# Optimization experiments

Hardware: AMD Instinct MI355X
Metric: run time of the kernel (lower is better)

The kernel has to match this reference:

```python
import jax, jax.numpy as jnp
import numpy as np

N = 50000
E = 800000
IN_C = 128
HID_C = 64
OUT_C = 64
HEADS = 4
NEG_SLOPE = 0.2


def setup_inputs() -> dict:
    key = jax.random.key(0)
    ks = jax.random.split(key, 12)
    x = jax.random.normal(ks[0], (N, IN_C), dtype=jnp.float32)
    edge_index = jax.random.randint(ks[1], (2, E), 0, N, dtype=jnp.int32)
    s = 0.1
    # layer 1 params (GATConv: shared lin for src/dst, att vectors per head, bias over H*C)
    W1 = jax.random.normal(ks[2], (IN_C, HEADS * HID_C), dtype=jnp.float32) * s
    att_src1 = jax.random.normal(ks[3], (HEADS, HID_C), dtype=jnp.float32) * s
    att_dst1 = jax.random.normal(ks[4], (HEADS, HID_C), dtype=jnp.float32) * s
    b1 = jnp.zeros((HEADS * HID_C,), dtype=jnp.float32)
    # layer 2 params
    W2 = jax.random.normal(ks[5], (HEADS * HID_C, HEADS * OUT_C), dtype=jnp.float32) * s
    att_src2 = jax.random.normal(ks[6], (HEADS, OUT_C), dtype=jnp.float32) * s
    att_dst2 = jax.random.normal(ks[7], (HEADS, OUT_C), dtype=jnp.float32) * s
    b2 = jnp.zeros((HEADS * OUT_C,), dtype=jnp.float32)
    return {"x": x, "edge_index": edge_index,
            "W1": W1, "att_src1": att_src1, "att_dst1": att_dst1, "b1": b1,
            "W2": W2, "att_src2": att_src2, "att_dst2": att_dst2, "b2": b2}


def _segment_softmax(e, dst, n):
    # e: [E, H], softmax over edges sharing the same dst node, per head
    m = jax.ops.segment_max(e, dst, num_segments=n)        # [N, H]
    ex = jnp.exp(e - m[dst])
    z = jax.ops.segment_sum(ex, dst, num_segments=n)       # [N, H]
    return ex / (z[dst] + 1e-16)


def _gat_layer(x, src, dst, W, att_src, att_dst, bias, heads, out_c):
    n = x.shape[0]
    h = (x @ W).reshape(n, heads, out_c)                   # [N, H, C]
    a_s = jnp.einsum('nhc,hc->nh', h, att_src)             # [N, H]
    a_d = jnp.einsum('nhc,hc->nh', h, att_dst)
    e = jax.nn.leaky_relu(a_s[src] + a_d[dst], NEG_SLOPE)  # [E, H]
    alpha = _segment_softmax(e, dst, n)                    # [E, H]
    msg = alpha[:, :, None] * h[src]                       # [E, H, C]
    out = jax.ops.segment_sum(msg, dst, num_segments=n)    # [N, H, C]
    return out.reshape(n, heads * out_c) + bias


def reference(x, edge_index, W1, att_src1, att_dst1, b1, W2, att_src2, att_dst2, b2):
    # PyG GATConv adds self-loops by default
    loops = jnp.arange(N, dtype=edge_index.dtype)
    src = jnp.concatenate([edge_index[0], loops])
    dst = jnp.concatenate([edge_index[1], loops])
    h = jax.nn.elu(_gat_layer(x, src, dst, W1, att_src1, att_dst1, b1, HEADS, HID_C))
    out = jax.nn.elu(_gat_layer(h, src, dst, W2, att_src2, att_dst2, b2, HEADS, OUT_C))
    return out  # [N, HEADS*OUT_C]
```

## Files before the change

kernel.cpp:

```cpp
#include <hip/hip_runtime.h>
#include <hip/hip_fp16.h>
#include <math.h>


#define LEAKY_SLOPE 0.2f

typedef __attribute__((ext_vector_type(8))) short short8v;
typedef __attribute__((ext_vector_type(4))) float float4v;


__global__ void hist_kernel(const int* __restrict__ ei, int* __restrict__ cnt,
                            int E, int Etot) {
    int e = blockIdx.x * blockDim.x + threadIdx.x;
    if (e >= Etot) return;
    int dst = (e < E) ? ei[E + e] : (e - E);
    atomicAdd(&cnt[dst], 1);
}

__global__ __launch_bounds__(1024) void scan_block(const int* __restrict__ cnt,
                                                   int* __restrict__ row_start,
                                                   int* __restrict__ partials,
                                                   int n) {
    __shared__ int wsum[16];
    int tid = threadIdx.x, lane = tid & 63, wid = tid >> 6;
    int gi = blockIdx.x * 1024 + tid;
    int v = (gi < n) ? cnt[gi] : 0;
    int x = v;
#pragma unroll
    for (int off = 1; off < 64; off <<= 1) {
        int y = __shfl_up(x, off, 64);
        if (lane >= off) x += y;
    }
    if (lane == 63) wsum[wid] = x;
    __syncthreads();
    if (wid == 0 && lane < 16) {
        int w = wsum[lane];
#pragma unroll
        for (int off = 1; off < 16; off <<= 1) {
            int y = __shfl_up(w, off, 16);
            if (lane >= off) w += y;
        }
        wsum[lane] = w;
    }
    __syncthreads();
    int excl = x - v + ((wid > 0) ? wsum[wid - 1] : 0);
    if (gi < n) row_start[gi] = excl;
    if (tid == 1023) partials[blockIdx.x] = wsum[15];
}

__global__ void scan_partials(int* __restrict__ partials, int nb) {
    int lane = threadIdx.x;
    int v = (lane < nb) ? partials[lane] : 0;
    int x = v;
#pragma unroll
    for (int off = 1; off < 64; off <<= 1) {
        int y = __shfl_up(x, off, 64);
        if (lane >= off) x += y;
    }
    if (lane < nb) partials[lane] = x - v;
    if (lane == nb - 1) partials[nb] = x;
}

__global__ __launch_bounds__(1024) void scan_add(int* __restrict__ row_start,
                                                 const int* __restrict__ partials,
                                                 int n, int nb) {
    int gi = blockIdx.x * 1024 + threadIdx.x;
    if (gi < n) row_start[gi] += partials[blockIdx.x];
    if (gi == 0) row_start[n] = partials[nb];
}

__global__ void scatter_kernel(const int* __restrict__ ei,
                               const int* __restrict__ row_start,
                               int* __restrict__ fill,
                               int2* __restrict__ edge_sd, int E, int Etot) {
    int e = blockIdx.x * blockDim.x + threadIdx.x;
    if (e >= Etot) return;
    int src, dst;
    if (e < E) { src = ei[e]; dst = ei[E + e]; }
    else       { src = e - E; dst = e - E; }
    int pos = row_start[dst] + atomicAdd(&fill[dst], 1);
    edge_sd[pos] = make_int2(src, dst);
}

__global__ void fill_rec(const int2* __restrict__ edge_sd,
                         const __half* __restrict__ a_s_h,
                         const float* __restrict__ a_d,
                         uint4* __restrict__ rec, int Etot) {
    int i = blockIdx.x * blockDim.x + threadIdx.x;
    if (i >= Etot) return;
    int2 sd = edge_sd[i];
    uint2 as2 = *(const uint2*)&a_s_h[(size_t)sd.x * 4];
    float4 ad4 = *(const float4*)&a_d[(size_t)sd.y * 4];
    float2 f01 = __half22float2(*(const __half2*)&as2.x);
    float2 f23 = __half22float2(*(const __half2*)&as2.y);
    float e0 = f01.x + ad4.x, e1 = f01.y + ad4.y;
    float e2 = f23.x + ad4.z, e3 = f23.y + ad4.w;
    e0 = (e0 > 0.f) ? e0 : LEAKY_SLOPE * e0;
    e1 = (e1 > 0.f) ? e1 : LEAKY_SLOPE * e1;
    e2 = (e2 > 0.f) ? e2 : LEAKY_SLOPE * e2;
    e3 = (e3 > 0.f) ? e3 : LEAKY_SLOPE * e3;
    __half2 w01 = __floats2half2_rn(__expf(e0), __expf(e1));
    __half2 w23 = __floats2half2_rn(__expf(e2), __expf(e3));
    uint4 r = {(unsigned)sd.x, *(unsigned*)&w01, *(unsigned*)&w23, 0u};
    rec[i] = r;
}


__device__ __forceinline__ short bf16_rne(float f) {
    unsigned u = __float_as_uint(f);
    return (short)((u + 0x7FFFu + ((u >> 16) & 1u)) >> 16);
}

__device__ __forceinline__ void split_bf16(float f, short& hi, short& lo) {
    unsigned u = __float_as_uint(f);
    hi = (short)(u >> 16);
    float fhi = __uint_as_float(u & 0xFFFF0000u);
    float flo = f - fhi;
    lo = (short)(__float_as_uint(flo) >> 16);
}

__global__ void split_B2(const float* __restrict__ W1, short* __restrict__ Bt1h,
                         short* __restrict__ Bt1l, const float* __restrict__ W2,
                         short* __restrict__ Bt2h, short* __restrict__ Bt2l) {
    int idx = blockIdx.x * 256 + threadIdx.x;
    if (idx < 128 * 256) {
        int k = idx >> 8, c = idx & 255;
        short hi, lo;
        split_bf16(W1[idx], hi, lo);
        Bt1h[c * 128 + k] = hi;
        Bt1l[c * 128 + k] = lo;
    } else {
        int j = idx - 128 * 256;
        int k = j >> 8, c = j & 255;
        short hi, lo;
        split_bf16(W2[j], hi, lo);
        Bt2h[c * 256 + k] = hi;
        Bt2l[c * 256 + k] = lo;
    }
}


template <int K, bool ABF16>
__global__ __launch_bounds__(256) void gemm_mfma(
    const void* __restrict__ Ap, const short* __restrict__ Bt_hi,
    const short* __restrict__ Bt_lo, __half* __restrict__ Ch,
    const float* __restrict__ att_src, const float* __restrict__ att_dst,
    __half* __restrict__ a_s_out, float* __restrict__ a_d_out, int M) {
    __shared__ short As_hi[128][40];
    __shared__ short Bs_hi[128][40];
    __shared__ short Bs_lo[128][40];

    const int col0 = (blockIdx.x & 1) * 128;
    const int row0 = (blockIdx.x >> 1) * 128;
    const int tid = threadIdx.x;
    const int lane = tid & 63;
    const int wave = tid >> 6;
    const int wr = wave >> 1, wc = wave & 1;
    const int quad = lane >> 4, lc = lane & 15;

    float4v acc[4][4] = {};

    for (int k0 = 0; k0 < K; k0 += 32) {
        if constexpr (ABF16) {
            const short* Abf = (const short*)Ap;
#pragma unroll
            for (int i = 0; i < 2; i++) {
                int slot = tid + i * 256;
                int r = slot >> 2;
                int ko = (slot & 3) * 8;
                short8v v = {};
                int gr = row0 + r;
                if (gr < M) v = *(const short8v*)&Abf[(size_t)gr * K + k0 + ko];
                *(short8v*)&As_hi[r][ko] = v;
            }
        } else {
            const float* A = (const float*)Ap;
#pragma unroll
            for (int i = 0; i < 4; i++) {
                int slot = tid + i * 256;
                int r = slot >> 3;
                int kq = (slot & 7) * 4;
                float4 v = {0.f, 0.f, 0.f, 0.f};
                int gr = row0 + r;
                if (gr < M) v = *(const float4*)&A[(size_t)gr * K + k0 + kq];
                short4 h4;
                h4.x = bf16_rne(v.x); h4.y = bf16_rne(v.y);
                h4.z = bf16_rne(v.z); h4.w = bf16_rne(v.w);
                *(short4*)&As_hi[r][kq] = h4;
            }
        }
#pragma unroll
        for (int i = 0; i < 2; i++) {
            int slot = tid + i * 256;
            int r = slot >> 2;
            int ko = (slot & 3) * 8;
            size_t gb = (size_t)(col0 + r) * K + k0 + ko;
            short8v vh = *(const short8v*)&Bt_hi[gb];
            short8v vl = *(const short8v*)&Bt_lo[gb];
            *(short8v*)&Bs_hi[r][ko] = vh;
            *(short8v*)&Bs_lo[r][ko] = vl;
        }
        __syncthreads();

        short8v a_hi[4], b_hi[4], b_lo[4];
#pragma unroll
        for (int mt = 0; mt < 4; mt++) {
            int r = wr * 64 + mt * 16 + lc;
            a_hi[mt] = *(const short8v*)&As_hi[r][quad * 8];
        }
#pragma unroll
        for (int nt = 0; nt < 4; nt++) {
            int n = wc * 64 + nt * 16 + lc;
            b_hi[nt] = *(const short8v*)&Bs_hi[n][quad * 8];
            b_lo[nt] = *(const short8v*)&Bs_lo[n][quad * 8];
        }
#pragma unroll
        for (int mt = 0; mt < 4; mt++)
#pragma unroll
            for (int nt = 0; nt < 4; nt++) {
                acc[mt][nt] = __builtin_amdgcn_mfma_f32_16x16x32_bf16(
                    a_hi[mt], b_hi[nt], acc[mt][nt], 0, 0, 0);
                acc[mt][nt] = __builtin_amdgcn_mfma_f32_16x16x32_bf16(
                    a_hi[mt], b_lo[nt], acc[mt][nt], 0, 0, 0);
            }
        __syncthreads();
    }

    const int head = (col0 >> 6) + wc;
    float as_c[4], ad_c[4];
#pragma unroll
    for (int nt = 0; nt < 4; nt++) {
        as_c[nt] = att_src[head * 64 + nt * 16 + lc];
        ad_c[nt] = att_dst[head * 64 + nt * 16 + lc];
    }

#pragma unroll
    for (int mt = 0; mt < 4; mt++) {
#pragma unroll
        for (int r = 0; r < 4; r++) {
            int gr = row0 + wr * 64 + mt * 16 + quad * 4 + r;
            float ps = 0.f, pd = 0.f;
#pragma unroll
            for (int nt = 0; nt < 4; nt++) {
                float c = acc[mt][nt][r];
                ps = fmaf(c, as_c[nt], ps);
                pd = fmaf(c, ad_c[nt], pd);
                if (gr < M)
                    Ch[(size_t)gr * 256 + col0 + wc * 64 + nt * 16 + lc] =
                        __float2half(c);
            }
#pragma unroll
            for (int off = 1; off < 16; off <<= 1) {
                ps += __shfl_xor(ps, off, 64);
                pd += __shfl_xor(pd, off, 64);
            }
            if (lc == 0 && gr < M) {
                a_s_out[gr * 4 + head] = __float2half(ps);
                a_d_out[gr * 4 + head] = pd;
            }
        }
    }
}


template <bool OUT_BF16>
__global__ __launch_bounds__(256) void gat_aggregate(
    const __half* __restrict__ hh, const uint4* __restrict__ rec,
    const int* __restrict__ row_start, const float* __restrict__ bias,
    void* __restrict__ outp, int n) {
    int node = (blockIdx.x * blockDim.x + threadIdx.x) >> 6;
    if (node >= n) return;
    int lane = threadIdx.x & 63;
    int half = lane >> 5, l32 = lane & 31;
    int head = l32 >> 3;

    int beg = row_start[node];
    int end = row_start[node + 1];
    int em1 = end - 1;

    float l = 0.f;
    float acc[8] = {};

    uint4 r0 = rec[min(beg + half, em1)];
    uint4 r1 = rec[min(beg + 2 + half, em1)];
    uint4 r2 = rec[min(beg + 4 + half, em1)];

#define GATH(rr) (*(const uint4*)&hh[(size_t)(rr).x * 256 + l32 * 8])
#define PROC(rr, vv, pp)                                                  \
    {                                                                     \
        unsigned u = (head & 2) ? (rr).z : (rr).y;                        \
        unsigned short us = (head & 1) ? (unsigned short)(u >> 16)        \
                                       : (unsigned short)(u & 0xFFFFu);   \
        float w = __half2float(*(const __half*)&us);                      \
        w = ((pp) + half < end) ? w : 0.f;                                \
        l += w;                                                           \
        const __half2* hp = (const __half2*)&(vv);                        \
        float2 f0 = __half22float2(hp[0]);                                \
        float2 f1 = __half22float2(hp[1]);                                \
        float2 f2 = __half22float2(hp[2]);                                \
        float2 f3 = __half22float2(hp[3]);                                \
        acc[0] = fmaf(w, f0.x, acc[0]); acc[1] = fmaf(w, f0.y, acc[1]);   \
        acc[2] = fmaf(w, f1.x, acc[2]); acc[3] = fmaf(w, f1.y, acc[3]);   \
        acc[4] = fmaf(w, f2.x, acc[4]); acc[5] = fmaf(w, f2.y, acc[5]);   \
        acc[6] = fmaf(w, f3.x, acc[6]); acc[7] = fmaf(w, f3.y, acc[7]);   \
    }

    uint4 h0 = GATH(r0);
    uint4 h1 = GATH(r1);
    uint4 h2;

    int p = beg;
    while (p < end) {
        h2 = GATH(r2);
        PROC(r0, h0, p);
        r0 = rec[min(p + 6 + half, em1)];
        p += 2;
        if (p >= end) break;
        h0 = GATH(r0);
        PROC(r1, h1, p);
        r1 = rec[min(p + 6 + half, em1)];
        p += 2;
        if (p >= end) break;
        h1 = GATH(r1);
        PROC(r2, h2, p);
        r2 = rec[min(p + 6 + half, em1)];
        p += 2;
    }
#undef GATH
#undef PROC

    l += __shfl_xor(l, 32);
#pragma unroll
    for (int j = 0; j < 8; j++) acc[j] += __shfl_xor(acc[j], 32);

    if (half == 0) {
        float rcp = 1.f / l;
        float4 b0 = *(const float4*)&bias[l32 * 8];
        float4 b1 = *(const float4*)&bias[l32 * 8 + 4];
        float o[8];
        o[0] = fmaf(acc[0], rcp, b0.x); o[1] = fmaf(acc[1], rcp, b0.y);
        o[2] = fmaf(acc[2], rcp, b0.z); o[3] = fmaf(acc[3], rcp, b0.w);
        o[4] = fmaf(acc[4], rcp, b1.x); o[5] = fmaf(acc[5], rcp, b1.y);
        o[6] = fmaf(acc[6], rcp, b1.z); o[7] = fmaf(acc[7], rcp, b1.w);
#pragma unroll
        for (int j = 0; j < 8; j++)
            o[j] = (o[j] > 0.f) ? o[j] : __expf(o[j]) - 1.f;
        if constexpr (OUT_BF16) {
            short ob[8];
#pragma unroll
            for (int j = 0; j < 8; j++) ob[j] = bf16_rne(o[j]);
            short* outb = (short*)outp;
            *(short4*)&outb[(size_t)node * 256 + l32 * 8] = *(short4*)&ob[0];
            *(short4*)&outb[(size_t)node * 256 + l32 * 8 + 4] = *(short4*)&ob[4];
        } else {
            float* outf = (float*)outp;
            *(float4*)&outf[(size_t)node * 256 + l32 * 8] = *(float4*)&o[0];
            *(float4*)&outf[(size_t)node * 256 + l32 * 8 + 4] = *(float4*)&o[4];
        }
    }
}


extern "C" void kernel_launch(void* const* d_in, const int* in_sizes, int n_in,
                              void* d_out, int out_size, void* d_ws, size_t ws_size,
                              hipStream_t stream) {
    const float* x   = (const float*)d_in[0];
    const int*   ei  = (const int*)d_in[1];
    const float* W1  = (const float*)d_in[2];
    const float* as1 = (const float*)d_in[3];
    const float* ad1 = (const float*)d_in[4];
    const float* b1  = (const float*)d_in[5];
    const float* W2  = (const float*)d_in[6];
    const float* as2 = (const float*)d_in[7];
    const float* ad2 = (const float*)d_in[8];
    const float* b2  = (const float*)d_in[9];
    float* out = (float*)d_out;

    const int N = in_sizes[0] / 128;
    const int E = in_sizes[1] / 2;
    const int Etot = E + N;
    const int NB = (N + 1023) / 1024;

    __half* h_half = (__half*)d_ws;
    short*  x1_bf  = (short*)(h_half + (size_t)N * 256);
    uint4*  rec    = (uint4*)(x1_bf + (size_t)N * 256);
    __half* a_s_h  = (__half*)(rec + Etot);
    float*  a_d    = (float*)(a_s_h + (size_t)N * 4);
    short*  Bt1h   = (short*)(a_d + (size_t)N * 4);
    short*  Bt1l   = Bt1h + 256 * 128;
    short*  Bt2h   = Bt1l + 256 * 128;
    short*  Bt2l   = Bt2h + 256 * 256;
    int*    cnt    = (int*)(Bt2l + 256 * 256);
    int*    fill   = cnt + N;
    int*    row_st = fill + N;
    int2*   edge_sd = (int2*)(row_st + (N + 2));
    int*    partials = (int*)(edge_sd + Etot);

    split_B2<<<384, 256, 0, stream>>>(W1, Bt1h, Bt1l, W2, Bt2h, Bt2l);

    hipMemsetAsync(cnt, 0, sizeof(int) * 2 * (size_t)N, stream);
    int eblocks = (Etot + 255) / 256;
    hist_kernel<<<eblocks, 256, 0, stream>>>(ei, cnt, E, Etot);
    scan_block<<<NB, 1024, 0, stream>>>(cnt, row_st, partials, N);
    scan_partials<<<1, 64, 0, stream>>>(partials, NB);
    scan_add<<<NB, 1024, 0, stream>>>(row_st, partials, N, NB);
    scatter_kernel<<<eblocks, 256, 0, stream>>>(ei, row_st, fill, edge_sd, E, Etot);

    dim3 ggrid(2 * ((N + 127) / 128));
    int ablocks = (N + 3) / 4;

    gemm_mfma<128, false><<<ggrid, 256, 0, stream>>>(x, Bt1h, Bt1l, h_half,
                                                     as1, ad1, a_s_h, a_d, N);
    fill_rec<<<eblocks, 256, 0, stream>>>(edge_sd, a_s_h, a_d, rec, Etot);
    gat_aggregate<true><<<ablocks, 256, 0, stream>>>(h_half, rec, row_st,
                                                     b1, x1_bf, N);
    gemm_mfma<256, true><<<ggrid, 256, 0, stream>>>(x1_bf, Bt2h, Bt2l, h_half,
                                                    as2, ad2, a_s_h, a_d, N);
    fill_rec<<<eblocks, 256, 0, stream>>>(edge_sd, a_s_h, a_d, rec, Etot);
    gat_aggregate<false><<<ablocks, 256, 0, stream>>>(h_half, rec, row_st,
                                                      b2, out, N);
}
```

Measured before the change: 402.1 us.

## Pad CSR rows to even length, fuse prep kernels, deepen aggregate prefetch

Each node's CSR row is padded to an even length. Padding slots are marked with src=-1 through a 0xFF memset and turned into zero-weight records in fill_rec. This lets the aggregation loop drop its bounds clamps and per-edge masking, and the gather pipeline goes from 3 to 4 records in flight. The weight split, the conversion of x to bf16 and the histogram are fused into one prep kernel, so the first GEMM reads bf16 input directly. The cost is extra padded records, an extra memset and wider fill_rec launches.

```diff
diff --git a/kernel.cpp b/kernel.cpp
--- a/kernel.cpp
+++ b/kernel.cpp
@@ -9,13 +9,59 @@
 typedef __attribute__((ext_vector_type(4))) float float4v;
 
 
-__global__ void hist_kernel(const int* __restrict__ ei, int* __restrict__ cnt,
-                            int E, int Etot) {
-    int e = blockIdx.x * blockDim.x + threadIdx.x;
-    if (e >= Etot) return;
-    int dst = (e < E) ? ei[E + e] : (e - E);
-    atomicAdd(&cnt[dst], 1);
-}
+__device__ __forceinline__ short bf16_rne(float f) {
+    unsigned u = __float_as_uint(f);
+    return (short)((u + 0x7FFFu + ((u >> 16) & 1u)) >> 16);
+}
+
+__device__ __forceinline__ void split_bf16(float f, short& hi, short& lo) {
+    unsigned u = __float_as_uint(f);
+    hi = (short)(u >> 16);
+    float fhi = __uint_as_float(u & 0xFFFF0000u);
+    float flo = f - fhi;
+    lo = (short)(__float_as_uint(flo) >> 16);
+}
+
+
+__global__ void prep_kernel(const float* __restrict__ W1, short* __restrict__ Bt1h,
+                            short* __restrict__ Bt1l, const float* __restrict__ W2,
+                            short* __restrict__ Bt2h, short* __restrict__ Bt2l,
+                            const float* __restrict__ x, short* __restrict__ x_bf,
+                            const int* __restrict__ ei, int* __restrict__ cnt,
+                            int E, int N, int xblocks) {
+    int b = blockIdx.x;
+    if (b < 128) {
+        int idx = b * 256 + threadIdx.x;
+        int k = idx >> 8, c = idx & 255;
+        short hi, lo;
+        split_bf16(W1[idx], hi, lo);
+        Bt1h[c * 128 + k] = hi;
+        Bt1l[c * 128 + k] = lo;
+    } else if (b < 384) {
+        int idx = (b - 128) * 256 + threadIdx.x;
+        int k = idx >> 8, c = idx & 255;
+        short hi, lo;
+        split_bf16(W2[idx], hi, lo);
+        Bt2h[c * 256 + k] = hi;
+        Bt2l[c * 256 + k] = lo;
+    } else if (b < 384 + xblocks) {
+        int t = (b - 384) * 256 + threadIdx.x;
+        if (t < N * 32) {
+            float4 v = *(const float4*)&x[(size_t)t * 4];
+            short4 h4;
+            h4.x = bf16_rne(v.x); h4.y = bf16_rne(v.y);
+            h4.z = bf16_rne(v.z); h4.w = bf16_rne(v.w);
+            *(short4*)&x_bf[(size_t)t * 4] = h4;
+        }
+    } else {
+        int e = (b - 384 - xblocks) * 256 + threadIdx.x;
+        if (e < E + N) {
+            int dst = (e < E) ? ei[E + e] : (e - E);
+            atomicAdd(&cnt[dst], 1);
+        }
+    }
+}
+
 
 __global__ __launch_bounds__(1024) void scan_block(const int* __restrict__ cnt,
                                                    int* __restrict__ row_start,
@@ -24,7 +70,7 @@
     __shared__ int wsum[16];
     int tid = threadIdx.x, lane = tid & 63, wid = tid >> 6;
     int gi = blockIdx.x * 1024 + tid;
-    int v = (gi < n) ? cnt[gi] : 0;
+    int v = (gi < n) ? ((cnt[gi] + 1) & ~1) : 0;
     int x = v;
 #pragma unroll
     for (int off = 1; off < 64; off <<= 1) {
@@ -85,10 +131,15 @@
 __global__ void fill_rec(const int2* __restrict__ edge_sd,
                          const __half* __restrict__ a_s_h,
                          const float* __restrict__ a_d,
-                         uint4* __restrict__ rec, int Etot) {
+                         uint4* __restrict__ rec, int EtotMax) {
     int i = blockIdx.x * blockDim.x + threadIdx.x;
-    if (i >= Etot) return;
+    if (i >= EtotMax) return;
     int2 sd = edge_sd[i];
+    if (sd.x < 0) {
+        uint4 z = {0u, 0u, 0u, 0u};
+        rec[i] = z;
+        return;
+    }
     uint2 as2 = *(const uint2*)&a_s_h[(size_t)sd.x * 4];
     float4 ad4 = *(const float4*)&a_d[(size_t)sd.y * 4];
     float2 f01 = __half22float2(*(const __half2*)&as2.x);
@@ -106,43 +157,9 @@
 }
 
 
-__device__ __forceinline__ short bf16_rne(float f) {
-    unsigned u = __float_as_uint(f);
-    return (short)((u + 0x7FFFu + ((u >> 16) & 1u)) >> 16);
-}
-
-__device__ __forceinline__ void split_bf16(float f, short& hi, short& lo) {
-    unsigned u = __float_as_uint(f);
-    hi = (short)(u >> 16);
-    float fhi = __uint_as_float(u & 0xFFFF0000u);
-    float flo = f - fhi;
-    lo = (short)(__float_as_uint(flo) >> 16);
-}
-
-__global__ void split_B2(const float* __restrict__ W1, short* __restrict__ Bt1h,
-                         short* __restrict__ Bt1l, const float* __restrict__ W2,
-                         short* __restrict__ Bt2h, short* __restrict__ Bt2l) {
-    int idx = blockIdx.x * 256 + threadIdx.x;
-    if (idx < 128 * 256) {
-        int k = idx >> 8, c = idx & 255;
-        short hi, lo;
-        split_bf16(W1[idx], hi, lo);
-        Bt1h[c * 128 + k] = hi;
-        Bt1l[c * 128 + k] = lo;
-    } else {
-        int j = idx - 128 * 256;
-        int k = j >> 8, c = j & 255;
-        short hi, lo;
-        split_bf16(W2[j], hi, lo);
-        Bt2h[c * 256 + k] = hi;
-        Bt2l[c * 256 + k] = lo;
-    }
-}
-
-
-template <int K, bool ABF16>
+template <int K>
 __global__ __launch_bounds__(256) void gemm_mfma(
-    const void* __restrict__ Ap, const short* __restrict__ Bt_hi,
+    const short* __restrict__ Abf, const short* __restrict__ Bt_hi,
     const short* __restrict__ Bt_lo, __half* __restrict__ Ch,
     const float* __restrict__ att_src, const float* __restrict__ att_dst,
     __half* __restrict__ a_s_out, float* __restrict__ a_d_out, int M) {
@@ -161,33 +178,15 @@
     float4v acc[4][4] = {};
 
     for (int k0 = 0; k0 < K; k0 += 32) {
-        if constexpr (ABF16) {
-            const short* Abf = (const short*)Ap;
-#pragma unroll
-            for (int i = 0; i < 2; i++) {
-                int slot = tid + i * 256;
-                int r = slot >> 2;
-                int ko = (slot & 3) * 8;
-                short8v v = {};
-                int gr = row0 + r;
-                if (gr < M) v = *(const short8v*)&Abf[(size_t)gr * K + k0 + ko];
-                *(short8v*)&As_hi[r][ko] = v;
-            }
-        } else {
-            const float* A = (const float*)Ap;
-#pragma unroll
-            for (int i = 0; i < 4; i++) {
-                int slot = tid + i * 256;
-                int r = slot >> 3;
-                int kq = (slot & 7) * 4;
-                float4 v = {0.f, 0.f, 0.f, 0.f};
-                int gr = row0 + r;
-                if (gr < M) v = *(const float4*)&A[(size_t)gr * K + k0 + kq];
-                short4 h4;
-                h4.x = bf16_rne(v.x); h4.y = bf16_rne(v.y);
-                h4.z = bf16_rne(v.z); h4.w = bf16_rne(v.w);
-                *(short4*)&As_hi[r][kq] = h4;
-            }
+#pragma unroll
+        for (int i = 0; i < 2; i++) {
+            int slot = tid + i * 256;
+            int r = slot >> 2;
+            int ko = (slot & 3) * 8;
+            short8v v = {};
+            int gr = row0 + r;
+            if (gr < M) v = *(const short8v*)&Abf[(size_t)gr * K + k0 + ko];
+            *(short8v*)&As_hi[r][ko] = v;
         }
 #pragma unroll
         for (int i = 0; i < 2; i++) {
@@ -273,26 +272,25 @@
     int lane = threadIdx.x & 63;
     int half = lane >> 5, l32 = lane & 31;
     int head = l32 >> 3;
+    unsigned wsh = (head & 1) << 4;
 
     int beg = row_start[node];
     int end = row_start[node + 1];
-    int em1 = end - 1;
 
     float l = 0.f;
     float acc[8] = {};
 
-    uint4 r0 = rec[min(beg + half, em1)];
-    uint4 r1 = rec[min(beg + 2 + half, em1)];
-    uint4 r2 = rec[min(beg + 4 + half, em1)];
+    uint4 r0 = rec[beg + half];
+    uint4 r1 = rec[beg + 2 + half];
+    uint4 r2 = rec[beg + 4 + half];
+    uint4 r3 = rec[beg + 6 + half];
 
 #define GATH(rr) (*(const uint4*)&hh[(size_t)(rr).x * 256 + l32 * 8])
-#define PROC(rr, vv, pp)                                                  \
+#define PROC(rr, vv)                                                      \
     {                                                                     \
         unsigned u = (head & 2) ? (rr).z : (rr).y;                        \
-        unsigned short us = (head & 1) ? (unsigned short)(u >> 16)        \
-                                       : (unsigned short)(u & 0xFFFFu);   \
+        unsigned short us = (unsigned short)(u >> wsh);                   \
         float w = __half2float(*(const __half*)&us);                      \
-        w = ((pp) + half < end) ? w : 0.f;                                \
         l += w;                                                           \
         const __half2* hp = (const __half2*)&(vv);                        \
         float2 f0 = __half22float2(hp[0]);                                \
@@ -307,23 +305,29 @@
 
     uint4 h0 = GATH(r0);
     uint4 h1 = GATH(r1);
-    uint4 h2;
+    uint4 h2 = GATH(r2);
+    uint4 h3;
 
     int p = beg;
     while (p < end) {
-        h2 = GATH(r2);
-        PROC(r0, h0, p);
-        r0 = rec[min(p + 6 + half, em1)];
+        h3 = GATH(r3);
+        PROC(r0, h0);
+        r0 = rec[p + 8 + half];
         p += 2;
         if (p >= end) break;
         h0 = GATH(r0);
-        PROC(r1, h1, p);
-        r1 = rec[min(p + 6 + half, em1)];
+        PROC(r1, h1);
+        r1 = rec[p + 8 + half];
         p += 2;
         if (p >= end) break;
         h1 = GATH(r1);
-        PROC(r2, h2, p);
-        r2 = rec[min(p + 6 + half, em1)];
+        PROC(r2, h2);
+        r2 = rec[p + 8 + half];
+        p += 2;
+        if (p >= end) break;
+        h2 = GATH(r2);
+        PROC(r3, h3);
+        r3 = rec[p + 8 + half];
         p += 2;
     }
 #undef GATH
@@ -379,12 +383,13 @@
     const int N = in_sizes[0] / 128;
     const int E = in_sizes[1] / 2;
     const int Etot = E + N;
+    const int EtotMax = Etot + N + 8;
     const int NB = (N + 1023) / 1024;
 
     __half* h_half = (__half*)d_ws;
     short*  x1_bf  = (short*)(h_half + (size_t)N * 256);
     uint4*  rec    = (uint4*)(x1_bf + (size_t)N * 256);
-    __half* a_s_h  = (__half*)(rec + Etot);
+    __half* a_s_h  = (__half*)(rec + EtotMax);
     float*  a_d    = (float*)(a_s_h + (size_t)N * 4);
     short*  Bt1h   = (short*)(a_d + (size_t)N * 4);
     short*  Bt1l   = Bt1h + 256 * 128;
@@ -394,13 +399,16 @@
     int*    fill   = cnt + N;
     int*    row_st = fill + N;
     int2*   edge_sd = (int2*)(row_st + (N + 2));
-    int*    partials = (int*)(edge_sd + Etot);
-
-    split_B2<<<384, 256, 0, stream>>>(W1, Bt1h, Bt1l, W2, Bt2h, Bt2l);
+    int*    partials = (int*)(edge_sd + EtotMax);
 
     hipMemsetAsync(cnt, 0, sizeof(int) * 2 * (size_t)N, stream);
-    int eblocks = (Etot + 255) / 256;
-    hist_kernel<<<eblocks, 256, 0, stream>>>(ei, cnt, E, Etot);
+    hipMemsetAsync(edge_sd, 0xFF, sizeof(int2) * (size_t)EtotMax, stream);
+
+    const int xblocks = (N * 32 + 255) / 256;
+    const int eblocks = (Etot + 255) / 256;
+    prep_kernel<<<384 + xblocks + eblocks, 256, 0, stream>>>(
+        W1, Bt1h, Bt1l, W2, Bt2h, Bt2l, x, x1_bf, ei, cnt, E, N, xblocks);
+
     scan_block<<<NB, 1024, 0, stream>>>(cnt, row_st, partials, N);
     scan_partials<<<1, 64, 0, stream>>>(partials, NB);
     scan_add<<<NB, 1024, 0, stream>>>(row_st, partials, N, NB);
@@ -408,15 +416,16 @@
 
     dim3 ggrid(2 * ((N + 127) / 128));
     int ablocks = (N + 3) / 4;
-
-    gemm_mfma<128, false><<<ggrid, 256, 0, stream>>>(x, Bt1h, Bt1l, h_half,
-                                                     as1, ad1, a_s_h, a_d, N);
-    fill_rec<<<eblocks, 256, 0, stream>>>(edge_sd, a_s_h, a_d, rec, Etot);
+    int fblocks = (EtotMax + 255) / 256;
+
+    gemm_mfma<128><<<ggrid, 256, 0, stream>>>(x1_bf, Bt1h, Bt1l, h_half,
+                                              as1, ad1, a_s_h, a_d, N);
+    fill_rec<<<fblocks, 256, 0, stream>>>(edge_sd, a_s_h, a_d, rec, EtotMax);
     gat_aggregate<true><<<ablocks, 256, 0, stream>>>(h_half, rec, row_st,
                                                      b1, x1_bf, N);
-    gemm_mfma<256, true><<<ggrid, 256, 0, stream>>>(x1_bf, Bt2h, Bt2l, h_half,
-                                                    as2, ad2, a_s_h, a_d, N);
-    fill_rec<<<eblocks, 256, 0, stream>>>(edge_sd, a_s_h, a_d, rec, Etot);
+    gemm_mfma<256><<<ggrid, 256, 0, stream>>>(x1_bf, Bt2h, Bt2l, h_half,
+                                              as2, ad2, a_s_h, a_d, N);
+    fill_rec<<<fblocks, 256, 0, stream>>>(edge_sd, a_s_h, a_d, rec, EtotMax);
     gat_aggregate<false><<<ablocks, 256, 0, stream>>>(h_half, rec, row_st,
                                                       b2, out, N);
 }
```

After: 400.8 us. About the same (-0.3%).
